# Kernel optimization log

Hardware: AMD Instinct MI355X
Metric: run time of the kernel (lower is better)

## Reference

```python
import jax, jax.numpy as jnp
import numpy as np

B, L, E, D1, D2 = 256, 128, 64, 512, 512


def setup_inputs() -> dict:
    key = jax.random.key(0)
    k1, k2, k3, kw = jax.random.split(key, 4)
    tensor1 = jax.random.normal(k1, (B, L, D1), dtype=jnp.float32)
    tensor2 = jax.random.normal(k2, (B, L, D2), dtype=jnp.float32)
    parameters_index = jax.random.randint(k3, (B,), 0, E, dtype=jnp.int32)
    # xavier_uniform with relu gain: gain*sqrt(6/(fan_in+fan_out)),
    # torch fan for [E,D1,D2]: fan_in = D1*D2, fan_out = E*D2
    gain = float(np.sqrt(2.0))
    bound = gain * float(np.sqrt(6.0 / (D1 * D2 + E * D2)))
    weights = jax.random.uniform(kw, (E, D1, D2), minval=-bound, maxval=bound, dtype=jnp.float32)
    return {"tensor1": tensor1, "tensor2": tensor2, "parameters_index": parameters_index, "weights": weights}


def reference(tensor1, tensor2, parameters_index, weights):
    # gather per-batch weight matrix [B, D1, D2], then bilinear form x1^T W x2
    w = weights[parameters_index]  # [B, D1, D2]
    # equals: sum over i,j of tensor1[b,l,i] * w[b,i,j] * tensor2[b,l,j] -> [B, L]
    return jnp.einsum('bli,bij,blj->bl', tensor1, w, tensor2)
```

## Files before the change

kernel.cpp:

```cpp
#include <hip/hip_runtime.h>
#include <stdint.h>

#define NB 256
#define NL 128
#define ND1 512
#define ND2 512

#define BI 256
#define BK 64
#define NKT (ND2 / BK)
#define LDST 72

typedef float float4_t __attribute__((ext_vector_type(4)));
typedef __bf16 bf16x8_t __attribute__((ext_vector_type(8)));
typedef unsigned short ushort4_t __attribute__((ext_vector_type(4)));
typedef unsigned short ushort8_t __attribute__((ext_vector_type(8)));

__device__ __forceinline__ unsigned short f2bf(float f) {
    unsigned int u = __float_as_uint(f);
    u += 0x7FFFu + ((u >> 16) & 1u);
    return (unsigned short)(u >> 16);
}

__device__ __forceinline__ ushort4_t cvt4(float4_t v) {
    ushort4_t u;
    u.x = f2bf(v.x); u.y = f2bf(v.y); u.z = f2bf(v.z); u.w = f2bf(v.w);
    return u;
}

__global__ __launch_bounds__(512, 4) void pdot_kernel(
    const float* __restrict__ t1, const float* __restrict__ t2,
    const int* __restrict__ pidx, const float* __restrict__ wgt,
    float* __restrict__ out)
{
    __shared__ unsigned short sA[NL * LDST];
    __shared__ unsigned short sB[BI * LDST];

    const int g  = blockIdx.x;
    const int b  = g & (NB - 1);
    const int it = g >> 8;
    const int i0 = it * BI;

    const int t  = threadIdx.x;
    const int w  = t >> 6;
    const int wv = w & 3;
    const int ih = w >> 2;
    const int ln = t & 63;
    const int nh = ln & 15;
    const int qd = ln >> 4;

    const int e = pidx[b];
    const float* aPtr  = t2  + (size_t)b * (NL * ND2);
    const float* bPtr  = wgt + (size_t)e * (ND1 * ND2) + (size_t)i0 * ND2;
    const float* t1p   = t1  + (size_t)b * (NL * ND1) + i0 + ih * 128;

    float4_t acc[2][8];
    #pragma unroll
    for (int i = 0; i < 2; ++i)
        #pragma unroll
        for (int j = 0; j < 8; ++j) {
            float4_t z = {0.f, 0.f, 0.f, 0.f};
            acc[i][j] = z;
        }

    const int s_row = t >> 4;
    const int s_kq  = (t & 15) * 4;
    const size_t sOff = (size_t)s_row * ND2 + s_kq;

    float4_t pa[4], pb[8];

    #pragma unroll
    for (int p = 0; p < 4; ++p)
        pa[p] = *(const float4_t*)(aPtr + sOff + (size_t)p * (32 * ND2));
    #pragma unroll
    for (int p = 0; p < 8; ++p)
        pb[p] = *(const float4_t*)(bPtr + sOff + (size_t)p * (32 * ND2));
    #pragma unroll
    for (int p = 0; p < 4; ++p) {
        const int row = p * 32 + s_row;
        *(ushort4_t*)(&sA[row * LDST + s_kq]) = cvt4(pa[p]);
    }
    #pragma unroll
    for (int p = 0; p < 8; ++p) {
        const int row = p * 32 + s_row;
        *(ushort4_t*)(&sB[row * LDST + s_kq]) = cvt4(pb[p]);
    }
    #pragma unroll
    for (int p = 0; p < 4; ++p)
        pa[p] = *(const float4_t*)(aPtr + sOff + BK + (size_t)p * (32 * ND2));
    #pragma unroll
    for (int p = 0; p < 8; ++p)
        pb[p] = *(const float4_t*)(bPtr + sOff + BK + (size_t)p * (32 * ND2));
    __builtin_amdgcn_sched_barrier(0);
    asm volatile("s_waitcnt lgkmcnt(0)" ::: "memory");
    __builtin_amdgcn_sched_barrier(0);
    __builtin_amdgcn_s_barrier();
    __builtin_amdgcn_sched_barrier(0);

    for (int kt = 0; kt < NKT; ++kt) {
        #pragma unroll
        for (int ks = 0; ks < 2; ++ks) {
            const int kf = ks * 32 + qd * 8;
            const int ra = wv * 32 + nh;
            bf16x8_t af0 = __builtin_bit_cast(bf16x8_t, *(ushort8_t*)(&sA[(ra     ) * LDST + kf]));
            bf16x8_t af1 = __builtin_bit_cast(bf16x8_t, *(ushort8_t*)(&sA[(ra + 16) * LDST + kf]));
            #pragma unroll
            for (int ns = 0; ns < 8; ++ns) {
                bf16x8_t bv = __builtin_bit_cast(bf16x8_t, *(ushort8_t*)(&sB[(ih * 128 + ns * 16 + nh) * LDST + kf]));
                acc[0][ns] = __builtin_amdgcn_mfma_f32_16x16x32_bf16(af0, bv, acc[0][ns], 0, 0, 0);
                acc[1][ns] = __builtin_amdgcn_mfma_f32_16x16x32_bf16(af1, bv, acc[1][ns], 0, 0, 0);
            }
        }

        if (kt < NKT - 1) {
            __builtin_amdgcn_sched_barrier(0);
            __builtin_amdgcn_s_barrier();
            __builtin_amdgcn_sched_barrier(0);

            #pragma unroll
            for (int p = 0; p < 4; ++p) {
                const int row = p * 32 + s_row;
                *(ushort4_t*)(&sA[row * LDST + s_kq]) = cvt4(pa[p]);
            }
            #pragma unroll
            for (int p = 0; p < 8; ++p) {
                const int row = p * 32 + s_row;
                *(ushort4_t*)(&sB[row * LDST + s_kq]) = cvt4(pb[p]);
            }
            if (kt < NKT - 2) {
                const size_t k0 = (size_t)(kt + 2) * BK;
                #pragma unroll
                for (int p = 0; p < 4; ++p)
                    pa[p] = *(const float4_t*)(aPtr + sOff + k0 + (size_t)p * (32 * ND2));
                #pragma unroll
                for (int p = 0; p < 8; ++p)
                    pb[p] = *(const float4_t*)(bPtr + sOff + k0 + (size_t)p * (32 * ND2));
            }
            __builtin_amdgcn_sched_barrier(0);
            asm volatile("s_waitcnt lgkmcnt(0)" ::: "memory");
            __builtin_amdgcn_sched_barrier(0);
            __builtin_amdgcn_s_barrier();
            __builtin_amdgcn_sched_barrier(0);
        }
    }

    #pragma unroll
    for (int ms = 0; ms < 2; ++ms) {
        #pragma unroll
        for (int r = 0; r < 4; ++r) {
            const int row = wv * 32 + ms * 16 + qd * 4 + r;
            float ps = 0.f;
            #pragma unroll
            for (int ns = 0; ns < 8; ++ns) {
                const float tv = t1p[(size_t)row * ND1 + ns * 16 + nh];
                ps += acc[ms][ns][r] * tv;
            }
            ps += __shfl_xor(ps, 1);
            ps += __shfl_xor(ps, 2);
            ps += __shfl_xor(ps, 4);
            ps += __shfl_xor(ps, 8);
            if (nh == 0) atomicAdd(&out[b * NL + row], ps);
        }
    }
}

extern "C" void kernel_launch(void* const* d_in, const int* in_sizes, int n_in,
                              void* d_out, int out_size, void* d_ws, size_t ws_size,
                              hipStream_t stream)
{
    const float* t1  = (const float*)d_in[0];
    const float* t2  = (const float*)d_in[1];
    const int* pidx  = (const int*)d_in[2];
    const float* wgt = (const float*)d_in[3];
    float* out = (float*)d_out;

    hipMemsetAsync(out, 0, (size_t)out_size * sizeof(float), stream);
    pdot_kernel<<<dim3(NB * (ND1 / BI)), dim3(512), 0, stream>>>(t1, t2, pidx, wgt, out);
}
```

Before: 220.1 us.

## Sort batches by expert index and remap blocks for weight cache reuse

Adds a small counting-sort kernel that builds a permutation grouping batch entries by their weight index. The main kernel then maps each block through this permutation, with a slot swizzle that places blocks sharing the same expert matrix on the same XCD (blockIdx mod 8), so reuse of the gathered weights in L2 can improve. It costs an extra kernel launch and a dependent load of perm per block, and it needs workspace. The old mapping is kept as a fallback.

New measurement: 218.3 us. No clear change (-0.8%).

```diff
diff --git a/kernel.cpp b/kernel.cpp
--- a/kernel.cpp
+++ b/kernel.cpp
@@ -5,6 +5,7 @@
 #define NL 128
 #define ND1 512
 #define ND2 512
+#define NE 64
 
 #define BI 256
 #define BK 64
@@ -28,16 +29,36 @@
     return u;
 }
 
+__global__ void sort_kernel(const int* __restrict__ pidx, int* __restrict__ perm)
+{
+    __shared__ int cnt[NE];
+    __shared__ int base[NE];
+    const int t = threadIdx.x;
+    if (t < NE) cnt[t] = 0;
+    __syncthreads();
+    const int e = pidx[t];
+    const int r = atomicAdd(&cnt[e], 1);
+    __syncthreads();
+    if (t == 0) {
+        int s = 0;
+        for (int i = 0; i < NE; ++i) { base[i] = s; s += cnt[i]; }
+    }
+    __syncthreads();
+    perm[base[e] + r] = t;
+}
+
+template <bool USE_PERM>
 __global__ __launch_bounds__(512, 4) void pdot_kernel(
     const float* __restrict__ t1, const float* __restrict__ t2,
     const int* __restrict__ pidx, const float* __restrict__ wgt,
-    float* __restrict__ out)
+    const int* __restrict__ perm, float* __restrict__ out)
 {
     __shared__ unsigned short sA[NL * LDST];
     __shared__ unsigned short sB[BI * LDST];
 
     const int g  = blockIdx.x;
-    const int b  = g & (NB - 1);
+    const int slot = (g & 7) * 32 + ((g >> 3) & 31);
+    const int b  = USE_PERM ? perm[slot] : (g & (NB - 1));
     const int it = g >> 8;
     const int i0 = it * BI;
 
@@ -175,5 +196,12 @@
     float* out = (float*)d_out;
 
     hipMemsetAsync(out, 0, (size_t)out_size * sizeof(float), stream);
-    pdot_kernel<<<dim3(NB * (ND1 / BI)), dim3(512), 0, stream>>>(t1, t2, pidx, wgt, out);
-}
+
+    if (ws_size >= NB * sizeof(int)) {
+        int* perm = (int*)d_ws;
+        sort_kernel<<<dim3(1), dim3(NB), 0, stream>>>(pidx, perm);
+        pdot_kernel<true><<<dim3(NB * (ND1 / BI)), dim3(512), 0, stream>>>(t1, t2, pidx, wgt, perm, out);
+    } else {
+        pdot_kernel<false><<<dim3(NB * (ND1 / BI)), dim3(512), 0, stream>>>(t1, t2, pidx, wgt, nullptr, out);
+    }
+}
```
